# Performance work log

Hardware: AMD Instinct MI355X
Metric: run time of the kernel (lower is better)

Reference implementation:

```python
import jax, jax.numpy as jnp
import numpy as np

N = 100000   # nodes
E = 1600000  # edges (avg degree 16)
D = 64       # in_dim == emb_dim
L = 3        # num_layers
G = 2000     # graphs in batch
LN_EPS = 1e-5


def setup_inputs() -> dict:
    key = jax.random.key(0)
    ks = jax.random.split(key, 14)
    s = 0.05  # xavier-ish small init scale
    x = jax.random.normal(ks[0], (N, D), jnp.float32)
    edge_index = jax.random.randint(ks[1], (2, E), 0, N, dtype=jnp.int32)
    batch = jnp.sort(jax.random.randint(ks[2], (N,), 0, G, dtype=jnp.int32))
    return {
        "x": x,
        "edge_index": edge_index,
        "batch": batch,
        # stacked per-layer GIN MLP params: Linear(D,D) -> SiLU -> Linear(D,D)
        "W1": jax.random.normal(ks[3], (L, D, D), jnp.float32) * s,
        "b1": jnp.zeros((L, D), jnp.float32),
        "W2": jax.random.normal(ks[4], (L, D, D), jnp.float32) * s,
        "b2": jnp.zeros((L, D), jnp.float32),
        "eps": jnp.zeros((L,), jnp.float32),  # trainable eps, init 0
        "ln_g": jnp.ones((L, D), jnp.float32),
        "ln_b": jnp.zeros((L, D), jnp.float32),
        # gate_nn: Linear(D, D//2) -> SiLU -> Linear(D//2, 1)
        "gw1": jax.random.normal(ks[5], (D, D // 2), jnp.float32) * s,
        "gb1": jnp.zeros((D // 2,), jnp.float32),
        "gw2": jax.random.normal(ks[6], (D // 2, 1), jnp.float32) * s,
        "gb2": jnp.zeros((1,), jnp.float32),
    }


def _layernorm(h, g, b):
    mu = jnp.mean(h, axis=-1, keepdims=True)
    var = jnp.mean(jnp.square(h - mu), axis=-1, keepdims=True)
    return (h - mu) * jax.lax.rsqrt(var + LN_EPS) * g + b


def reference(x, edge_index, batch, W1, b1, W2, b2, eps, ln_g, ln_b, gw1, gb1, gw2, gb2):
    src, dst = edge_index[0], edge_index[1]
    # ---- GIN layers (eval mode: dropout is identity) ----
    for l in range(L):
        agg = jax.ops.segment_sum(x[src], dst, num_segments=N)  # scatter-add of neighbor feats
        h = (1.0 + eps[l]) * x + agg                             # GIN update
        h = jax.nn.silu(h @ W1[l] + b1[l]) @ W2[l] + b2[l]       # 2-layer MLP
        x = _layernorm(h, ln_g[l], ln_b[l])
    # ---- GlobalAttention pooling ----
    gate = (jax.nn.silu(x @ gw1 + gb1) @ gw2 + gb2)[:, 0]        # [N]
    m = jax.ops.segment_max(gate, batch, num_segments=G)         # per-graph max for stability
    e = jnp.exp(gate - m[batch])
    denom = jax.ops.segment_sum(e, batch, num_segments=G)
    a = e / denom[batch]                                         # per-graph softmax
    out = jax.ops.segment_sum(a[:, None] * x, batch, num_segments=G)  # [G, D]
    return out
```

## Files before the change

### kernel.cpp

```cpp
#include <hip/hip_runtime.h>
#include <math.h>

#define NN 100000
#define NE 1600000
#define D 64
#define NG 2000
#define LN_EPS 1e-5f
#define NB ((NN + 255) / 256)
#define NBK NB
#define NTILE ((NN + 63) / 64)
#define EPB 6400
#define LSTR 72
#define WFRAG_MLP 24576
#define WFRAG_TOT 26624

typedef __attribute__((ext_vector_type(8))) short short8;
typedef __attribute__((ext_vector_type(4))) float floatx4;

__device__ __forceinline__ unsigned short f2bf(float f) {
    unsigned int u = __float_as_uint(f);
    u += 0x7FFF + ((u >> 16) & 1);
    return (unsigned short)(u >> 16);
}
__device__ __forceinline__ float bfu2f(unsigned short v) {
    return __uint_as_float(((unsigned int)v) << 16);
}

__global__ __launch_bounds__(256) void k_conv(const float* __restrict__ x,
                                              unsigned short* __restrict__ xb) {
    int i = blockIdx.x * 256 + threadIdx.x;
    xb[i] = f2bf(x[i]);
}

__global__ __launch_bounds__(256) void k_wprep(const float* __restrict__ W1,
                                               const float* __restrict__ W2,
                                               const float* __restrict__ gw1,
                                               unsigned short* __restrict__ wfrag) {
    int idx = blockIdx.x * 256 + threadIdx.x;
    if (idx < WFRAG_MLP) {
        int l = idx / 8192;
        int rem = idx % 8192;
        int mat = rem / 4096;
        int r2 = rem % 4096;
        int ks = r2 / 2048;
        int c = (r2 / 512) % 4;
        int lane = (r2 / 8) % 64;
        int j = r2 % 8;
        int n = lane & 15, q = lane >> 4;
        int k = ks * 32 + q * 8 + j;
        int col = c * 16 + n;
        const float* Wm = mat ? W2 : W1;
        wfrag[idx] = f2bf(Wm[l * 4096 + k * 64 + col]);
    } else if (idx < WFRAG_TOT) {
        int g = idx - WFRAG_MLP;
        int ks = g / 1024;
        int c = (g / 512) % 2;
        int lane = (g / 8) % 64;
        int j = g % 8;
        int n = lane & 15, q = lane >> 4;
        int k = ks * 32 + q * 8 + j;
        wfrag[idx] = f2bf(gw1[k * 32 + c * 16 + n]);
    }
}

__global__ __launch_bounds__(256) void k_bcount(const int* __restrict__ dst,
                                                int* __restrict__ btot) {
    __shared__ int lcnt[NBK];
    int e0 = blockIdx.x * EPB;
    int tid = threadIdx.x;
    for (int i = tid; i < NBK; i += 256) lcnt[i] = 0;
    __syncthreads();
    for (int k = 0; k < EPB; k += 256)
        atomicAdd(&lcnt[dst[e0 + k + tid] >> 8], 1);
    __syncthreads();
    for (int i = tid; i < NBK; i += 256) {
        int c = lcnt[i];
        if (c) atomicAdd(&btot[i], c);
    }
}

__global__ __launch_bounds__(512) void k_bscan(const int* __restrict__ btot,
                                               int* __restrict__ bbase) {
    __shared__ int s[512];
    int t = threadIdx.x;
    int v = (t < NB) ? btot[t] : 0;
    s[t] = v;
    __syncthreads();
    for (int off = 1; off < 512; off <<= 1) {
        int u = (t >= off) ? s[t - off] : 0;
        __syncthreads();
        s[t] += u;
        __syncthreads();
    }
    if (t < NB) bbase[t] = s[t] - v;
    if (t == NB - 1) bbase[NB] = s[t];
}

__global__ __launch_bounds__(512) void k_bcurinit(const int* __restrict__ bbase,
                                                  int* __restrict__ bcur,
                                                  int* __restrict__ row_ptr) {
    int b = threadIdx.x;
    if (b < NBK) bcur[b * 16] = bbase[b];
    if (b == 0) row_ptr[NN] = NE;
}

__global__ __launch_bounds__(256) void k_part(const int* __restrict__ src,
                                              const int* __restrict__ dst,
                                              int* __restrict__ bcur,
                                              unsigned int* __restrict__ tmp) {
    __shared__ int lcnt[NBK];
    __shared__ int lbase[NBK];
    __shared__ int sd[EPB];
    __shared__ int ss[EPB];
    int e0 = blockIdx.x * EPB;
    int tid = threadIdx.x;

    for (int i = tid; i < NBK; i += 256) lcnt[i] = 0;
    __syncthreads();

    for (int k = 0; k < EPB; k += 256) {
        int d = dst[e0 + k + tid];
        int s = src[e0 + k + tid];
        sd[k + tid] = d;
        ss[k + tid] = s;
        atomicAdd(&lcnt[d >> 8], 1);
    }
    __syncthreads();

    for (int i = tid; i < NBK; i += 256) {
        int c = lcnt[i];
        lbase[i] = c ? atomicAdd(&bcur[i * 16], c) : 0;
        lcnt[i] = 0;
    }
    __syncthreads();

    for (int k = 0; k < EPB; k += 256) {
        int d = sd[k + tid];
        int s = ss[k + tid];
        int b = d >> 8;
        int pos = lbase[b] + atomicAdd(&lcnt[b], 1);
        tmp[pos] = ((unsigned int)s << 8) | (unsigned int)(d & 255);
    }
}

__global__ __launch_bounds__(256) void k_bfill(const unsigned int* __restrict__ tmp,
                                               const int* __restrict__ bbase,
                                               int* __restrict__ row_ptr,
                                               int* __restrict__ col) {
    __shared__ int lcur[256];
    __shared__ int wsum[4];
    int b = blockIdx.x;
    int nb0 = b * 256;
    int nodes = min(256, NN - nb0);
    int tid = threadIdx.x;
    int lane = tid & 63;
    int w = tid >> 6;
    int estart = bbase[b], eend = bbase[b + 1];

    lcur[tid] = 0;
    __syncthreads();
    for (int e = estart + tid; e < eend; e += 256)
        atomicAdd(&lcur[tmp[e] & 255], 1);
    __syncthreads();

    int v = lcur[tid];
    int x = v;
#pragma unroll
    for (int off = 1; off < 64; off <<= 1) {
        int u = __shfl_up(x, off, 64);
        if (lane >= off) x += u;
    }
    if (lane == 63) wsum[w] = x;
    __syncthreads();
    int base = estart;
    for (int k = 0; k < w; k++) base += wsum[k];
    int rp = base + x - v;
    if (tid < nodes) row_ptr[nb0 + tid] = rp;
    lcur[tid] = rp;
    __syncthreads();

    for (int e = estart + tid; e < eend; e += 256) {
        unsigned int p = tmp[e];
        int pos = atomicAdd(&lcur[p & 255], 1);
        col[pos] = (int)(p >> 8);
    }
}

__global__ __launch_bounds__(256) void k_gather(const unsigned short* __restrict__ xin,
                                                unsigned short* __restrict__ h,
                                                const int* __restrict__ row_ptr,
                                                const int* __restrict__ col,
                                                const float* __restrict__ epsp) {
    int w = threadIdx.x >> 6;
    int lane = threadIdx.x & 63;
    int g = lane >> 4;
    int fl = lane & 15;
    int node = (blockIdx.x * 4 + w) * 4 + g;
    int start = row_ptr[node], end = row_ptr[node + 1];

    float4 A0 = {0, 0, 0, 0}, A1 = {0, 0, 0, 0}, A2 = {0, 0, 0, 0}, A3 = {0, 0, 0, 0};
    int eb = start;
    for (; eb + 16 <= end; eb += 16) {
        int c = col[eb + fl];
        ushort4 v[16];
#pragma unroll
        for (int j = 0; j < 16; j++) {
            int idx = __shfl(c, g * 16 + j, 64);
            v[j] = *(const ushort4*)(xin + ((size_t)idx << 6) + fl * 4);
        }
#pragma unroll
        for (int j = 0; j < 16; j += 4) {
            A0.x += bfu2f(v[j].x); A0.y += bfu2f(v[j].y); A0.z += bfu2f(v[j].z); A0.w += bfu2f(v[j].w);
            A1.x += bfu2f(v[j+1].x); A1.y += bfu2f(v[j+1].y); A1.z += bfu2f(v[j+1].z); A1.w += bfu2f(v[j+1].w);
            A2.x += bfu2f(v[j+2].x); A2.y += bfu2f(v[j+2].y); A2.z += bfu2f(v[j+2].z); A2.w += bfu2f(v[j+2].w);
            A3.x += bfu2f(v[j+3].x); A3.y += bfu2f(v[j+3].y); A3.z += bfu2f(v[j+3].z); A3.w += bfu2f(v[j+3].w);
        }
    }
    if (eb < end) {
        int cnt = end - eb;
        int c = (fl < cnt) ? col[eb + fl] : 0;
        int j = 0;
        for (; j + 4 <= cnt; j += 4) {
            int i0 = __shfl(c, g * 16 + j, 64);
            int i1 = __shfl(c, g * 16 + j + 1, 64);
            int i2 = __shfl(c, g * 16 + j + 2, 64);
            int i3 = __shfl(c, g * 16 + j + 3, 64);
            ushort4 v0 = *(const ushort4*)(xin + ((size_t)i0 << 6) + fl * 4);
            ushort4 v1 = *(const ushort4*)(xin + ((size_t)i1 << 6) + fl * 4);
            ushort4 v2 = *(const ushort4*)(xin + ((size_t)i2 << 6) + fl * 4);
            ushort4 v3 = *(const ushort4*)(xin + ((size_t)i3 << 6) + fl * 4);
            A0.x += bfu2f(v0.x); A0.y += bfu2f(v0.y); A0.z += bfu2f(v0.z); A0.w += bfu2f(v0.w);
            A1.x += bfu2f(v1.x); A1.y += bfu2f(v1.y); A1.z += bfu2f(v1.z); A1.w += bfu2f(v1.w);
            A2.x += bfu2f(v2.x); A2.y += bfu2f(v2.y); A2.z += bfu2f(v2.z); A2.w += bfu2f(v2.w);
            A3.x += bfu2f(v3.x); A3.y += bfu2f(v3.y); A3.z += bfu2f(v3.z); A3.w += bfu2f(v3.w);
        }
        for (; j < cnt; j++) {
            int i0 = __shfl(c, g * 16 + j, 64);
            ushort4 v0 = *(const ushort4*)(xin + ((size_t)i0 << 6) + fl * 4);
            A0.x += bfu2f(v0.x); A0.y += bfu2f(v0.y); A0.z += bfu2f(v0.z); A0.w += bfu2f(v0.w);
        }
    }
    float ev = 1.0f + *epsp;
    ushort4 xs = *(const ushort4*)(xin + ((size_t)node << 6) + fl * 4);
    ushort4 o;
    o.x = f2bf(ev * bfu2f(xs.x) + ((A0.x + A1.x) + (A2.x + A3.x)));
    o.y = f2bf(ev * bfu2f(xs.y) + ((A0.y + A1.y) + (A2.y + A3.y)));
    o.z = f2bf(ev * bfu2f(xs.z) + ((A0.z + A1.z) + (A2.z + A3.z)));
    o.w = f2bf(ev * bfu2f(xs.w) + ((A0.w + A1.w) + (A2.w + A3.w)));
    *(ushort4*)(h + ((size_t)node << 6) + fl * 4) = o;
}

template <int LAST>
__global__ __launch_bounds__(256) void k_mfma(const unsigned short* __restrict__ h,
                                              unsigned short* __restrict__ xout,
                                              const short8* __restrict__ wf,
                                              const short8* __restrict__ gf,
                                              const float* __restrict__ b1,
                                              const float* __restrict__ b2,
                                              const float* __restrict__ lng,
                                              const float* __restrict__ lnb,
                                              const float* __restrict__ gb1,
                                              const float* __restrict__ gw2,
                                              const float* __restrict__ gb2,
                                              float* __restrict__ gate) {
    __shared__ __align__(16) unsigned short a2[4][16 * LSTR];
    int w = threadIdx.x >> 6;
    int lane = threadIdx.x & 63;
    int n = lane & 15;
    int q = lane >> 4;
    int base = blockIdx.x * 64 + w * 16;

    short8 B1f[2][4], B2f[2][4];
#pragma unroll
    for (int ks = 0; ks < 2; ks++)
#pragma unroll
        for (int c = 0; c < 4; c++) {
            B1f[ks][c] = wf[(ks * 4 + c) * 64 + lane];
            B2f[ks][c] = wf[512 + (ks * 4 + c) * 64 + lane];
        }
    short8 B3f[2][2];
    if (LAST) {
#pragma unroll
        for (int ks = 0; ks < 2; ks++)
#pragma unroll
            for (int c = 0; c < 2; c++)
                B3f[ks][c] = gf[(ks * 2 + c) * 64 + lane];
    }

    float b1v[4], b2v[4], lgv[4], lbv[4];
#pragma unroll
    for (int c = 0; c < 4; c++) {
        b1v[c] = b1[c * 16 + n];
        b2v[c] = b2[c * 16 + n];
        lgv[c] = lng[c * 16 + n];
        lbv[c] = lnb[c * 16 + n];
    }
    float gb1v[2], gw2v[2], gb2v = 0.f;
    if (LAST) {
        gb1v[0] = gb1[n]; gb1v[1] = gb1[16 + n];
        gw2v[0] = gw2[n]; gw2v[1] = gw2[16 + n];
        gb2v = gb2[0];
    }

    unsigned short* aw = a2[w];

    int mnode = base + n;
    int mc = min(mnode, NN - 1);
    const short8* hp = (const short8*)(h + ((size_t)mc << 6));
    short8 A0 = hp[q];
    short8 A1 = hp[4 + q];

    floatx4 acc1[4];
#pragma unroll
    for (int c = 0; c < 4; c++) {
        floatx4 a = {b1v[c], b1v[c], b1v[c], b1v[c]};
        a = __builtin_amdgcn_mfma_f32_16x16x32_bf16(A0, B1f[0][c], a, 0, 0, 0);
        a = __builtin_amdgcn_mfma_f32_16x16x32_bf16(A1, B1f[1][c], a, 0, 0, 0);
        acc1[c] = a;
    }

#pragma unroll
    for (int c = 0; c < 4; c++)
#pragma unroll
        for (int r = 0; r < 4; r++) {
            float v = acc1[c][r];
            v = v / (1.0f + __expf(-v));
            aw[(q * 4 + r) * LSTR + c * 16 + n] = f2bf(v);
        }

    const short8* ap = (const short8*)(aw + n * LSTR);
    short8 A20 = ap[q];
    short8 A21 = ap[4 + q];

    floatx4 acc2[4];
#pragma unroll
    for (int c = 0; c < 4; c++) {
        floatx4 a = {b2v[c], b2v[c], b2v[c], b2v[c]};
        a = __builtin_amdgcn_mfma_f32_16x16x32_bf16(A20, B2f[0][c], a, 0, 0, 0);
        a = __builtin_amdgcn_mfma_f32_16x16x32_bf16(A21, B2f[1][c], a, 0, 0, 0);
        acc2[c] = a;
    }

    float mu[4], inv[4];
#pragma unroll
    for (int r = 0; r < 4; r++) {
        float s = acc2[0][r] + acc2[1][r] + acc2[2][r] + acc2[3][r];
#pragma unroll
        for (int off = 1; off < 16; off <<= 1) s += __shfl_xor(s, off, 64);
        mu[r] = s * (1.0f / 64.0f);
        float d0 = acc2[0][r] - mu[r], d1 = acc2[1][r] - mu[r];
        float d2 = acc2[2][r] - mu[r], d3 = acc2[3][r] - mu[r];
        float vv = d0 * d0 + d1 * d1 + d2 * d2 + d3 * d3;
#pragma unroll
        for (int off = 1; off < 16; off <<= 1) vv += __shfl_xor(vv, off, 64);
        inv[r] = rsqrtf(vv * (1.0f / 64.0f) + LN_EPS);
    }

#pragma unroll
    for (int c = 0; c < 4; c++)
#pragma unroll
        for (int r = 0; r < 4; r++) {
            int node = base + q * 4 + r;
            float o = (acc2[c][r] - mu[r]) * inv[r] * lgv[c] + lbv[c];
            unsigned short ob = f2bf(o);
            if (node < NN) xout[((size_t)node << 6) + c * 16 + n] = ob;
            if (LAST) aw[(q * 4 + r) * LSTR + c * 16 + n] = ob;
        }

    if (LAST) {
        const short8* gp = (const short8*)(aw + n * LSTR);
        short8 G0 = gp[q];
        short8 G1 = gp[4 + q];
        floatx4 acc3[2];
#pragma unroll
        for (int c = 0; c < 2; c++) {
            floatx4 a = {gb1v[c], gb1v[c], gb1v[c], gb1v[c]};
            a = __builtin_amdgcn_mfma_f32_16x16x32_bf16(G0, B3f[0][c], a, 0, 0, 0);
            a = __builtin_amdgcn_mfma_f32_16x16x32_bf16(G1, B3f[1][c], a, 0, 0, 0);
            acc3[c] = a;
        }
#pragma unroll
        for (int r = 0; r < 4; r++) {
            float v0 = acc3[0][r];
            v0 = v0 / (1.0f + __expf(-v0));
            float v1 = acc3[1][r];
            v1 = v1 / (1.0f + __expf(-v1));
            float gsum = v0 * gw2v[0] + v1 * gw2v[1];
#pragma unroll
            for (int off = 1; off < 16; off <<= 1) gsum += __shfl_xor(gsum, off, 64);
            int node = base + q * 4 + r;
            if (n == 0 && node < NN) gate[node] = gsum + gb2v;
        }
    }
}

__global__ __launch_bounds__(256) void k_pool(const unsigned short* __restrict__ xf,
                                              const float* __restrict__ gate,
                                              const int* __restrict__ batch,
                                              float* __restrict__ out) {
    __shared__ float redm[4];
    __shared__ float reds[4];
    __shared__ float racc[4][D];
    int g = blockIdx.x;
    int w = threadIdx.x >> 6;
    int lane = threadIdx.x & 63;

    int lo = 0, hi = NN;
    while (lo < hi) { int mid = (lo + hi) >> 1; if (batch[mid] < g) lo = mid + 1; else hi = mid; }
    int start = lo;
    hi = NN;
    while (lo < hi) { int mid = (lo + hi) >> 1; if (batch[mid] < g + 1) lo = mid + 1; else hi = mid; }
    int end = lo;

    if (start >= end) {
        if (w == 0) out[((size_t)g << 6) + lane] = 0.0f;
        return;
    }

    float m = -INFINITY;
    for (int i = start + (int)threadIdx.x; i < end; i += 256) m = fmaxf(m, gate[i]);
#pragma unroll
    for (int mm = 32; mm >= 1; mm >>= 1) m = fmaxf(m, __shfl_xor(m, mm, 64));
    if (lane == 0) redm[w] = m;
    __syncthreads();
    m = fmaxf(fmaxf(redm[0], redm[1]), fmaxf(redm[2], redm[3]));

    float s = 0.0f;
    for (int i = start + (int)threadIdx.x; i < end; i += 256) s += __expf(gate[i] - m);
#pragma unroll
    for (int mm = 32; mm >= 1; mm >>= 1) s += __shfl_xor(s, mm, 64);
    if (lane == 0) reds[w] = s;
    __syncthreads();
    s = (reds[0] + reds[1]) + (reds[2] + reds[3]);

    float acc = 0.0f;
    for (int i = start + w; i < end; i += 4)
        acc += __expf(gate[i] - m) * bfu2f(xf[((size_t)i << 6) + lane]);
    racc[w][lane] = acc;
    __syncthreads();
    if (w == 0)
        out[((size_t)g << 6) + lane] =
            ((racc[0][lane] + racc[1][lane]) + (racc[2][lane] + racc[3][lane])) / s;
}

extern "C" void kernel_launch(void* const* d_in, const int* in_sizes, int n_in,
                              void* d_out, int out_size, void* d_ws, size_t ws_size,
                              hipStream_t stream) {
    const float* x   = (const float*)d_in[0];
    const int* ei    = (const int*)d_in[1];
    const int* batch = (const int*)d_in[2];
    const float* W1  = (const float*)d_in[3];
    const float* b1  = (const float*)d_in[4];
    const float* W2  = (const float*)d_in[5];
    const float* b2  = (const float*)d_in[6];
    const float* eps = (const float*)d_in[7];
    const float* lng = (const float*)d_in[8];
    const float* lnb = (const float*)d_in[9];
    const float* gw1 = (const float*)d_in[10];
    const float* gb1 = (const float*)d_in[11];
    const float* gw2 = (const float*)d_in[12];
    const float* gb2 = (const float*)d_in[13];

    const int* src = ei;
    const int* dst = ei + NE;

    unsigned short* xb    = (unsigned short*)d_ws;
    unsigned short* h     = xb + (size_t)NN * D;
    float* gate           = (float*)(h + (size_t)NN * D);
    int* row_ptr          = (int*)(gate + NN);
    int* col              = row_ptr + NN + 1;
    unsigned int* tmp     = (unsigned int*)(col + NE);
    int* btot             = (int*)(tmp + NE);
    int* bbase            = btot + NB;
    int* bcur             = bbase + NB + 1;
    unsigned short* wfrag = (unsigned short*)(bcur + NBK * 16);

    float* out = (float*)d_out;

    hipMemsetAsync(btot, 0, (size_t)NB * sizeof(int), stream);
    k_conv<<<(NN * D) / 256, 256, 0, stream>>>(x, xb);
    k_wprep<<<WFRAG_TOT / 256, 256, 0, stream>>>(W1, W2, gw1, wfrag);
    k_bcount<<<NE / EPB, 256, 0, stream>>>(dst, btot);
    k_bscan<<<1, 512, 0, stream>>>(btot, bbase);
    k_bcurinit<<<1, 512, 0, stream>>>(bbase, bcur, row_ptr);
    k_part<<<NE / EPB, 256, 0, stream>>>(src, dst, bcur, tmp);
    k_bfill<<<NBK, 256, 0, stream>>>(tmp, bbase, row_ptr, col);

    const short8* wf0 = (const short8*)(wfrag);
    const short8* wf1 = (const short8*)(wfrag + 8192);
    const short8* wf2 = (const short8*)(wfrag + 16384);
    const short8* gf  = (const short8*)(wfrag + WFRAG_MLP);

    k_gather<<<NN / 16, 256, 0, stream>>>(xb, h, row_ptr, col, eps + 0);
    k_mfma<0><<<NTILE, 256, 0, stream>>>(h, xb, wf0, gf,
        b1 + 0 * D, b2 + 0 * D, lng + 0 * D, lnb + 0 * D, gb1, gw2, gb2, gate);

    k_gather<<<NN / 16, 256, 0, stream>>>(xb, h, row_ptr, col, eps + 1);
    k_mfma<0><<<NTILE, 256, 0, stream>>>(h, xb, wf1, gf,
        b1 + 1 * D, b2 + 1 * D, lng + 1 * D, lnb + 1 * D, gb1, gw2, gb2, gate);

    k_gather<<<NN / 16, 256, 0, stream>>>(xb, h, row_ptr, col, eps + 2);
    k_mfma<1><<<NTILE, 256, 0, stream>>>(h, xb, wf2, gf,
        b1 + 2 * D, b2 + 2 * D, lng + 2 * D, lnb + 2 * D, gb1, gw2, gb2, gate);

    k_pool<<<NG, 256, 0, stream>>>(xb, gate, batch, out);
}
```

Measured before the change: 336.6 us.

## Fuse neighbor gather into MLP layer kernel and drop fp32-to-bf16 conversion pass

Merges the per-layer gather/aggregate kernel into the MFMA MLP kernel. Aggregated rows are written to shared memory instead of a global h buffer, and output ping-pongs between two bf16 buffers. The first layer gathers directly from fp32 x, which removes the separate conversion kernel. The bcur init is folded into the scan kernel. Together these cut launches and the global round trip of h, but the first layer now gathers twice as many bytes per edge, and gathers run with only 4 nodes per wave-group per iteration, which may lower memory-level parallelism.

```diff
diff --git a/kernel.cpp b/kernel.cpp
--- a/kernel.cpp
+++ b/kernel.cpp
@@ -24,12 +24,6 @@
 }
 __device__ __forceinline__ float bfu2f(unsigned short v) {
     return __uint_as_float(((unsigned int)v) << 16);
-}
-
-__global__ __launch_bounds__(256) void k_conv(const float* __restrict__ x,
-                                              unsigned short* __restrict__ xb) {
-    int i = blockIdx.x * 256 + threadIdx.x;
-    xb[i] = f2bf(x[i]);
 }
 
 __global__ __launch_bounds__(256) void k_wprep(const float* __restrict__ W1,
@@ -80,7 +74,9 @@
 }
 
 __global__ __launch_bounds__(512) void k_bscan(const int* __restrict__ btot,
-                                               int* __restrict__ bbase) {
+                                               int* __restrict__ bbase,
+                                               int* __restrict__ bcur,
+                                               int* __restrict__ row_ptr) {
     __shared__ int s[512];
     int t = threadIdx.x;
     int v = (t < NB) ? btot[t] : 0;
@@ -92,16 +88,12 @@
         s[t] += u;
         __syncthreads();
     }
-    if (t < NB) bbase[t] = s[t] - v;
+    if (t < NB) {
+        bbase[t] = s[t] - v;
+        bcur[t * 16] = s[t] - v;
+    }
     if (t == NB - 1) bbase[NB] = s[t];
-}
-
-__global__ __launch_bounds__(512) void k_bcurinit(const int* __restrict__ bbase,
-                                                  int* __restrict__ bcur,
-                                                  int* __restrict__ row_ptr) {
-    int b = threadIdx.x;
-    if (b < NBK) bcur[b * 16] = bbase[b];
-    if (b == 0) row_ptr[NN] = NE;
+    if (t == 0) row_ptr[NN] = NE;
 }
 
 __global__ __launch_bounds__(256) void k_part(const int* __restrict__ src,
@@ -186,89 +178,106 @@
     }
 }
 
-__global__ __launch_bounds__(256) void k_gather(const unsigned short* __restrict__ xin,
-                                                unsigned short* __restrict__ h,
-                                                const int* __restrict__ row_ptr,
-                                                const int* __restrict__ col,
-                                                const float* __restrict__ epsp) {
-    int w = threadIdx.x >> 6;
-    int lane = threadIdx.x & 63;
-    int g = lane >> 4;
-    int fl = lane & 15;
-    int node = (blockIdx.x * 4 + w) * 4 + g;
-    int start = row_ptr[node], end = row_ptr[node + 1];
-
-    float4 A0 = {0, 0, 0, 0}, A1 = {0, 0, 0, 0}, A2 = {0, 0, 0, 0}, A3 = {0, 0, 0, 0};
-    int eb = start;
-    for (; eb + 16 <= end; eb += 16) {
-        int c = col[eb + fl];
-        ushort4 v[16];
-#pragma unroll
-        for (int j = 0; j < 16; j++) {
-            int idx = __shfl(c, g * 16 + j, 64);
-            v[j] = *(const ushort4*)(xin + ((size_t)idx << 6) + fl * 4);
-        }
-#pragma unroll
-        for (int j = 0; j < 16; j += 4) {
-            A0.x += bfu2f(v[j].x); A0.y += bfu2f(v[j].y); A0.z += bfu2f(v[j].z); A0.w += bfu2f(v[j].w);
-            A1.x += bfu2f(v[j+1].x); A1.y += bfu2f(v[j+1].y); A1.z += bfu2f(v[j+1].z); A1.w += bfu2f(v[j+1].w);
-            A2.x += bfu2f(v[j+2].x); A2.y += bfu2f(v[j+2].y); A2.z += bfu2f(v[j+2].z); A2.w += bfu2f(v[j+2].w);
-            A3.x += bfu2f(v[j+3].x); A3.y += bfu2f(v[j+3].y); A3.z += bfu2f(v[j+3].z); A3.w += bfu2f(v[j+3].w);
-        }
-    }
-    if (eb < end) {
-        int cnt = end - eb;
-        int c = (fl < cnt) ? col[eb + fl] : 0;
-        int j = 0;
-        for (; j + 4 <= cnt; j += 4) {
-            int i0 = __shfl(c, g * 16 + j, 64);
-            int i1 = __shfl(c, g * 16 + j + 1, 64);
-            int i2 = __shfl(c, g * 16 + j + 2, 64);
-            int i3 = __shfl(c, g * 16 + j + 3, 64);
-            ushort4 v0 = *(const ushort4*)(xin + ((size_t)i0 << 6) + fl * 4);
-            ushort4 v1 = *(const ushort4*)(xin + ((size_t)i1 << 6) + fl * 4);
-            ushort4 v2 = *(const ushort4*)(xin + ((size_t)i2 << 6) + fl * 4);
-            ushort4 v3 = *(const ushort4*)(xin + ((size_t)i3 << 6) + fl * 4);
-            A0.x += bfu2f(v0.x); A0.y += bfu2f(v0.y); A0.z += bfu2f(v0.z); A0.w += bfu2f(v0.w);
-            A1.x += bfu2f(v1.x); A1.y += bfu2f(v1.y); A1.z += bfu2f(v1.z); A1.w += bfu2f(v1.w);
-            A2.x += bfu2f(v2.x); A2.y += bfu2f(v2.y); A2.z += bfu2f(v2.z); A2.w += bfu2f(v2.w);
-            A3.x += bfu2f(v3.x); A3.y += bfu2f(v3.y); A3.z += bfu2f(v3.z); A3.w += bfu2f(v3.w);
-        }
-        for (; j < cnt; j++) {
-            int i0 = __shfl(c, g * 16 + j, 64);
-            ushort4 v0 = *(const ushort4*)(xin + ((size_t)i0 << 6) + fl * 4);
-            A0.x += bfu2f(v0.x); A0.y += bfu2f(v0.y); A0.z += bfu2f(v0.z); A0.w += bfu2f(v0.w);
-        }
-    }
-    float ev = 1.0f + *epsp;
-    ushort4 xs = *(const ushort4*)(xin + ((size_t)node << 6) + fl * 4);
-    ushort4 o;
-    o.x = f2bf(ev * bfu2f(xs.x) + ((A0.x + A1.x) + (A2.x + A3.x)));
-    o.y = f2bf(ev * bfu2f(xs.y) + ((A0.y + A1.y) + (A2.y + A3.y)));
-    o.z = f2bf(ev * bfu2f(xs.z) + ((A0.z + A1.z) + (A2.z + A3.z)));
-    o.w = f2bf(ev * bfu2f(xs.w) + ((A0.w + A1.w) + (A2.w + A3.w)));
-    *(ushort4*)(h + ((size_t)node << 6) + fl * 4) = o;
-}
-
-template <int LAST>
-__global__ __launch_bounds__(256) void k_mfma(const unsigned short* __restrict__ h,
-                                              unsigned short* __restrict__ xout,
-                                              const short8* __restrict__ wf,
-                                              const short8* __restrict__ gf,
-                                              const float* __restrict__ b1,
-                                              const float* __restrict__ b2,
-                                              const float* __restrict__ lng,
-                                              const float* __restrict__ lnb,
-                                              const float* __restrict__ gb1,
-                                              const float* __restrict__ gw2,
-                                              const float* __restrict__ gb2,
-                                              float* __restrict__ gate) {
+template <int FIRST, int LAST>
+__global__ __launch_bounds__(256) void k_layer(const float* __restrict__ xf32,
+                                               const unsigned short* __restrict__ xbf,
+                                               unsigned short* __restrict__ xout,
+                                               const int* __restrict__ row_ptr,
+                                               const int* __restrict__ col,
+                                               const float* __restrict__ epsp,
+                                               const short8* __restrict__ wf,
+                                               const short8* __restrict__ gf,
+                                               const float* __restrict__ b1,
+                                               const float* __restrict__ b2,
+                                               const float* __restrict__ lng,
+                                               const float* __restrict__ lnb,
+                                               const float* __restrict__ gb1,
+                                               const float* __restrict__ gw2,
+                                               const float* __restrict__ gb2,
+                                               float* __restrict__ gate) {
     __shared__ __align__(16) unsigned short a2[4][16 * LSTR];
     int w = threadIdx.x >> 6;
     int lane = threadIdx.x & 63;
     int n = lane & 15;
     int q = lane >> 4;
+    int g = q;
+    int fl = n;
     int base = blockIdx.x * 64 + w * 16;
+    unsigned short* aw = a2[w];
+
+    float ev = 1.0f + *epsp;
+
+    for (int sub = 0; sub < 4; sub++) {
+        int node = base + sub * 4 + g;
+        int nc = min(node, NN - 1);
+        int start = row_ptr[nc], end = row_ptr[nc + 1];
+
+        float4 A0 = {0, 0, 0, 0}, A1 = {0, 0, 0, 0}, A2 = {0, 0, 0, 0}, A3 = {0, 0, 0, 0};
+        int eb = start;
+        for (; eb + 16 <= end; eb += 16) {
+            int c = col[eb + fl];
+            if (FIRST) {
+#pragma unroll
+                for (int half = 0; half < 2; half++) {
+                    float4 v[8];
+#pragma unroll
+                    for (int j = 0; j < 8; j++) {
+                        int idx = __shfl(c, g * 16 + half * 8 + j, 64);
+                        v[j] = *(const float4*)(xf32 + ((size_t)idx << 6) + fl * 4);
+                    }
+#pragma unroll
+                    for (int j = 0; j < 8; j += 4) {
+                        A0.x += v[j].x;   A0.y += v[j].y;   A0.z += v[j].z;   A0.w += v[j].w;
+                        A1.x += v[j+1].x; A1.y += v[j+1].y; A1.z += v[j+1].z; A1.w += v[j+1].w;
+                        A2.x += v[j+2].x; A2.y += v[j+2].y; A2.z += v[j+2].z; A2.w += v[j+2].w;
+                        A3.x += v[j+3].x; A3.y += v[j+3].y; A3.z += v[j+3].z; A3.w += v[j+3].w;
+                    }
+                }
+            } else {
+                ushort4 v[16];
+#pragma unroll
+                for (int j = 0; j < 16; j++) {
+                    int idx = __shfl(c, g * 16 + j, 64);
+                    v[j] = *(const ushort4*)(xbf + ((size_t)idx << 6) + fl * 4);
+                }
+#pragma unroll
+                for (int j = 0; j < 16; j += 4) {
+                    A0.x += bfu2f(v[j].x);   A0.y += bfu2f(v[j].y);   A0.z += bfu2f(v[j].z);   A0.w += bfu2f(v[j].w);
+                    A1.x += bfu2f(v[j+1].x); A1.y += bfu2f(v[j+1].y); A1.z += bfu2f(v[j+1].z); A1.w += bfu2f(v[j+1].w);
+                    A2.x += bfu2f(v[j+2].x); A2.y += bfu2f(v[j+2].y); A2.z += bfu2f(v[j+2].z); A2.w += bfu2f(v[j+2].w);
+                    A3.x += bfu2f(v[j+3].x); A3.y += bfu2f(v[j+3].y); A3.z += bfu2f(v[j+3].z); A3.w += bfu2f(v[j+3].w);
+                }
+            }
+        }
+        if (eb < end) {
+            int cnt = end - eb;
+            int c = (fl < cnt) ? col[eb + fl] : 0;
+            for (int j = 0; j < cnt; j++) {
+                int idx = __shfl(c, g * 16 + j, 64);
+                if (FIRST) {
+                    float4 v0 = *(const float4*)(xf32 + ((size_t)idx << 6) + fl * 4);
+                    A0.x += v0.x; A0.y += v0.y; A0.z += v0.z; A0.w += v0.w;
+                } else {
+                    ushort4 v0 = *(const ushort4*)(xbf + ((size_t)idx << 6) + fl * 4);
+                    A0.x += bfu2f(v0.x); A0.y += bfu2f(v0.y); A0.z += bfu2f(v0.z); A0.w += bfu2f(v0.w);
+                }
+            }
+        }
+        float sx, sy, sz, sw;
+        if (FIRST) {
+            float4 xs = *(const float4*)(xf32 + ((size_t)nc << 6) + fl * 4);
+            sx = xs.x; sy = xs.y; sz = xs.z; sw = xs.w;
+        } else {
+            ushort4 xs = *(const ushort4*)(xbf + ((size_t)nc << 6) + fl * 4);
+            sx = bfu2f(xs.x); sy = bfu2f(xs.y); sz = bfu2f(xs.z); sw = bfu2f(xs.w);
+        }
+        ushort4 o;
+        o.x = f2bf(ev * sx + ((A0.x + A1.x) + (A2.x + A3.x)));
+        o.y = f2bf(ev * sy + ((A0.y + A1.y) + (A2.y + A3.y)));
+        o.z = f2bf(ev * sz + ((A0.z + A1.z) + (A2.z + A3.z)));
+        o.w = f2bf(ev * sw + ((A0.w + A1.w) + (A2.w + A3.w)));
+        *(ushort4*)(aw + (sub * 4 + g) * LSTR + fl * 4) = o;
+    }
 
     short8 B1f[2][4], B2f[2][4];
 #pragma unroll
@@ -302,13 +311,9 @@
         gb2v = gb2[0];
     }
 
-    unsigned short* aw = a2[w];
-
-    int mnode = base + n;
-    int mc = min(mnode, NN - 1);
-    const short8* hp = (const short8*)(h + ((size_t)mc << 6));
-    short8 A0 = hp[q];
-    short8 A1 = hp[4 + q];
+    const short8* ap = (const short8*)(aw + n * LSTR);
+    short8 A0 = ap[q];
+    short8 A1 = ap[4 + q];
 
     floatx4 acc1[4];
 #pragma unroll
@@ -328,7 +333,6 @@
             aw[(q * 4 + r) * LSTR + c * 16 + n] = f2bf(v);
         }
 
-    const short8* ap = (const short8*)(aw + n * LSTR);
     short8 A20 = ap[q];
     short8 A21 = ap[4 + q];
 
@@ -368,9 +372,8 @@
         }
 
     if (LAST) {
-        const short8* gp = (const short8*)(aw + n * LSTR);
-        short8 G0 = gp[q];
-        short8 G1 = gp[4 + q];
+        short8 G0 = ap[q];
+        short8 G1 = ap[4 + q];
         floatx4 acc3[2];
 #pragma unroll
         for (int c = 0; c < 2; c++) {
@@ -464,9 +467,9 @@
     const int* src = ei;
     const int* dst = ei + NE;
 
-    unsigned short* xb    = (unsigned short*)d_ws;
-    unsigned short* h     = xb + (size_t)NN * D;
-    float* gate           = (float*)(h + (size_t)NN * D);
+    unsigned short* xa    = (unsigned short*)d_ws;
+    unsigned short* xbuf  = xa + (size_t)NN * D;
+    float* gate           = (float*)(xbuf + (size_t)NN * D);
     int* row_ptr          = (int*)(gate + NN);
     int* col              = row_ptr + NN + 1;
     unsigned int* tmp     = (unsigned int*)(col + NE);
@@ -478,11 +481,9 @@
     float* out = (float*)d_out;
 
     hipMemsetAsync(btot, 0, (size_t)NB * sizeof(int), stream);
-    k_conv<<<(NN * D) / 256, 256, 0, stream>>>(x, xb);
     k_wprep<<<WFRAG_TOT / 256, 256, 0, stream>>>(W1, W2, gw1, wfrag);
     k_bcount<<<NE / EPB, 256, 0, stream>>>(dst, btot);
-    k_bscan<<<1, 512, 0, stream>>>(btot, bbase);
-    k_bcurinit<<<1, 512, 0, stream>>>(bbase, bcur, row_ptr);
+    k_bscan<<<1, 512, 0, stream>>>(btot, bbase, bcur, row_ptr);
     k_part<<<NE / EPB, 256, 0, stream>>>(src, dst, bcur, tmp);
     k_bfill<<<NBK, 256, 0, stream>>>(tmp, bbase, row_ptr, col);
 
@@ -491,17 +492,12 @@
     const short8* wf2 = (const short8*)(wfrag + 16384);
     const short8* gf  = (const short8*)(wfrag + WFRAG_MLP);
 
-    k_gather<<<NN / 16, 256, 0, stream>>>(xb, h, row_ptr, col, eps + 0);
-    k_mfma<0><<<NTILE, 256, 0, stream>>>(h, xb, wf0, gf,
-        b1 + 0 * D, b2 + 0 * D, lng + 0 * D, lnb + 0 * D, gb1, gw2, gb2, gate);
-
-    k_gather<<<NN / 16, 256, 0, stream>>>(xb, h, row_ptr, col, eps + 1);
-    k_mfma<0><<<NTILE, 256, 0, stream>>>(h, xb, wf1, gf,
-        b1 + 1 * D, b2 + 1 * D, lng + 1 * D, lnb + 1 * D, gb1, gw2, gb2, gate);
-
-    k_gather<<<NN / 16, 256, 0, stream>>>(xb, h, row_ptr, col, eps + 2);
-    k_mfma<1><<<NTILE, 256, 0, stream>>>(h, xb, wf2, gf,
-        b1 + 2 * D, b2 + 2 * D, lng + 2 * D, lnb + 2 * D, gb1, gw2, gb2, gate);
-
-    k_pool<<<NG, 256, 0, stream>>>(xb, gate, batch, out);
-}
+    k_layer<1, 0><<<NTILE, 256, 0, stream>>>(x, nullptr, xa, row_ptr, col, eps + 0,
+        wf0, gf, b1 + 0 * D, b2 + 0 * D, lng + 0 * D, lnb + 0 * D, gb1, gw2, gb2, gate);
+    k_layer<0, 0><<<NTILE, 256, 0, stream>>>(nullptr, xa, xbuf, row_ptr, col, eps + 1,
+        wf1, gf, b1 + 1 * D, b2 + 1 * D, lng + 1 * D, lnb + 1 * D, gb1, gw2, gb2, gate);
+    k_layer<0, 1><<<NTILE, 256, 0, stream>>>(nullptr, xbuf, xa, row_ptr, col, eps + 2,
+        wf2, gf, b1 + 2 * D, b2 + 2 * D, lng + 2 * D, lnb + 2 * D, gb1, gw2, gb2, gate);
+
+    k_pool<<<NG, 256, 0, stream>>>(xa, gate, batch, out);
+}
```

Result: slower. 452.4 us (+34.4%).

## Build CSR with fixed-capacity buckets, dropping the count and scan passes

Applied to the files above, without the earlier changes.

Replaces the count / scan / partition / fill CSR construction with fixed-capacity per-bucket regions (CAP slots per 256-node bucket). This removes the dst counting kernel, the scan kernel, the memset and their launches. The fill kernel now stages each bucket in shared memory and sorts it in place, writing separate start and end row pointers that the gather kernel reads. It relies on no bucket exceeding CAP edges, which holds for uniform random graphs but could overflow on skewed degree distributions. A small edit also reuses an existing LDS pointer for the gate MFMA operands.

```diff
diff --git a/kernel.cpp b/kernel.cpp
--- a/kernel.cpp
+++ b/kernel.cpp
@@ -10,6 +10,7 @@
 #define NBK NB
 #define NTILE ((NN + 63) / 64)
 #define EPB 6400
+#define CAP 6144
 #define LSTR 72
 #define WFRAG_MLP 24576
 #define WFRAG_TOT 26624
@@ -63,51 +64,15 @@
     }
 }
 
-__global__ __launch_bounds__(256) void k_bcount(const int* __restrict__ dst,
-                                                int* __restrict__ btot) {
-    __shared__ int lcnt[NBK];
-    int e0 = blockIdx.x * EPB;
-    int tid = threadIdx.x;
-    for (int i = tid; i < NBK; i += 256) lcnt[i] = 0;
-    __syncthreads();
-    for (int k = 0; k < EPB; k += 256)
-        atomicAdd(&lcnt[dst[e0 + k + tid] >> 8], 1);
-    __syncthreads();
-    for (int i = tid; i < NBK; i += 256) {
-        int c = lcnt[i];
-        if (c) atomicAdd(&btot[i], c);
-    }
-}
-
-__global__ __launch_bounds__(512) void k_bscan(const int* __restrict__ btot,
-                                               int* __restrict__ bbase) {
-    __shared__ int s[512];
-    int t = threadIdx.x;
-    int v = (t < NB) ? btot[t] : 0;
-    s[t] = v;
-    __syncthreads();
-    for (int off = 1; off < 512; off <<= 1) {
-        int u = (t >= off) ? s[t - off] : 0;
-        __syncthreads();
-        s[t] += u;
-        __syncthreads();
-    }
-    if (t < NB) bbase[t] = s[t] - v;
-    if (t == NB - 1) bbase[NB] = s[t];
-}
-
-__global__ __launch_bounds__(512) void k_bcurinit(const int* __restrict__ bbase,
-                                                  int* __restrict__ bcur,
-                                                  int* __restrict__ row_ptr) {
+__global__ __launch_bounds__(512) void k_init(int* __restrict__ bcur) {
     int b = threadIdx.x;
-    if (b < NBK) bcur[b * 16] = bbase[b];
-    if (b == 0) row_ptr[NN] = NE;
+    if (b < NBK) bcur[b * 16] = b * CAP;
 }
 
 __global__ __launch_bounds__(256) void k_part(const int* __restrict__ src,
                                               const int* __restrict__ dst,
                                               int* __restrict__ bcur,
-                                              unsigned int* __restrict__ tmp) {
+                                              unsigned int* __restrict__ colbuf) {
     __shared__ int lcnt[NBK];
     __shared__ int lbase[NBK];
     __shared__ int sd[EPB];
@@ -139,28 +104,32 @@
         int s = ss[k + tid];
         int b = d >> 8;
         int pos = lbase[b] + atomicAdd(&lcnt[b], 1);
-        tmp[pos] = ((unsigned int)s << 8) | (unsigned int)(d & 255);
-    }
-}
-
-__global__ __launch_bounds__(256) void k_bfill(const unsigned int* __restrict__ tmp,
-                                               const int* __restrict__ bbase,
-                                               int* __restrict__ row_ptr,
-                                               int* __restrict__ col) {
+        colbuf[pos] = ((unsigned int)s << 8) | (unsigned int)(d & 255);
+    }
+}
+
+__global__ __launch_bounds__(256) void k_bfill(unsigned int* __restrict__ colbuf,
+                                               const int* __restrict__ bcur,
+                                               int* __restrict__ rps,
+                                               int* __restrict__ rpe) {
+    __shared__ unsigned int sld[CAP];
     __shared__ int lcur[256];
     __shared__ int wsum[4];
     int b = blockIdx.x;
+    int ebase = b * CAP;
+    int cnt = bcur[b * 16] - ebase;
     int nb0 = b * 256;
     int nodes = min(256, NN - nb0);
     int tid = threadIdx.x;
     int lane = tid & 63;
     int w = tid >> 6;
-    int estart = bbase[b], eend = bbase[b + 1];
-
+
+    for (int e = tid; e < cnt; e += 256) sld[e] = colbuf[ebase + e];
     lcur[tid] = 0;
     __syncthreads();
-    for (int e = estart + tid; e < eend; e += 256)
-        atomicAdd(&lcur[tmp[e] & 255], 1);
+
+    for (int e = tid; e < cnt; e += 256)
+        atomicAdd(&lcur[sld[e] & 255], 1);
     __syncthreads();
 
     int v = lcur[tid];
@@ -172,23 +141,27 @@
     }
     if (lane == 63) wsum[w] = x;
     __syncthreads();
-    int base = estart;
+    int base = ebase;
     for (int k = 0; k < w; k++) base += wsum[k];
     int rp = base + x - v;
-    if (tid < nodes) row_ptr[nb0 + tid] = rp;
+    if (tid < nodes) {
+        rps[nb0 + tid] = rp;
+        rpe[nb0 + tid] = rp + v;
+    }
     lcur[tid] = rp;
     __syncthreads();
 
-    for (int e = estart + tid; e < eend; e += 256) {
-        unsigned int p = tmp[e];
+    for (int e = tid; e < cnt; e += 256) {
+        unsigned int p = sld[e];
         int pos = atomicAdd(&lcur[p & 255], 1);
-        col[pos] = (int)(p >> 8);
+        colbuf[pos] = p >> 8;
     }
 }
 
 __global__ __launch_bounds__(256) void k_gather(const unsigned short* __restrict__ xin,
                                                 unsigned short* __restrict__ h,
-                                                const int* __restrict__ row_ptr,
+                                                const int* __restrict__ rps,
+                                                const int* __restrict__ rpe,
                                                 const int* __restrict__ col,
                                                 const float* __restrict__ epsp) {
     int w = threadIdx.x >> 6;
@@ -196,7 +169,7 @@
     int g = lane >> 4;
     int fl = lane & 15;
     int node = (blockIdx.x * 4 + w) * 4 + g;
-    int start = row_ptr[node], end = row_ptr[node + 1];
+    int start = rps[node], end = rpe[node];
 
     float4 A0 = {0, 0, 0, 0}, A1 = {0, 0, 0, 0}, A2 = {0, 0, 0, 0}, A3 = {0, 0, 0, 0};
     int eb = start;
@@ -368,9 +341,8 @@
         }
 
     if (LAST) {
-        const short8* gp = (const short8*)(aw + n * LSTR);
-        short8 G0 = gp[q];
-        short8 G1 = gp[4 + q];
+        short8 G0 = ap[q];
+        short8 G1 = ap[4 + q];
         floatx4 acc3[2];
 #pragma unroll
         for (int c = 0; c < 2; c++) {
@@ -467,39 +439,34 @@
     unsigned short* xb    = (unsigned short*)d_ws;
     unsigned short* h     = xb + (size_t)NN * D;
     float* gate           = (float*)(h + (size_t)NN * D);
-    int* row_ptr          = (int*)(gate + NN);
-    int* col              = row_ptr + NN + 1;
-    unsigned int* tmp     = (unsigned int*)(col + NE);
-    int* btot             = (int*)(tmp + NE);
-    int* bbase            = btot + NB;
-    int* bcur             = bbase + NB + 1;
+    int* rps              = (int*)(gate + NN);
+    int* rpe              = rps + NN;
+    int* colbuf           = rpe + NN;
+    int* bcur             = colbuf + (size_t)NBK * CAP;
     unsigned short* wfrag = (unsigned short*)(bcur + NBK * 16);
 
     float* out = (float*)d_out;
 
-    hipMemsetAsync(btot, 0, (size_t)NB * sizeof(int), stream);
     k_conv<<<(NN * D) / 256, 256, 0, stream>>>(x, xb);
     k_wprep<<<WFRAG_TOT / 256, 256, 0, stream>>>(W1, W2, gw1, wfrag);
-    k_bcount<<<NE / EPB, 256, 0, stream>>>(dst, btot);
-    k_bscan<<<1, 512, 0, stream>>>(btot, bbase);
-    k_bcurinit<<<1, 512, 0, stream>>>(bbase, bcur, row_ptr);
-    k_part<<<NE / EPB, 256, 0, stream>>>(src, dst, bcur, tmp);
-    k_bfill<<<NBK, 256, 0, stream>>>(tmp, bbase, row_ptr, col);
+    k_init<<<1, 512, 0, stream>>>(bcur);
+    k_part<<<NE / EPB, 256, 0, stream>>>(src, dst, bcur, (unsigned int*)colbuf);
+    k_bfill<<<NBK, 256, 0, stream>>>((unsigned int*)colbuf, bcur, rps, rpe);
 
     const short8* wf0 = (const short8*)(wfrag);
     const short8* wf1 = (const short8*)(wfrag + 8192);
     const short8* wf2 = (const short8*)(wfrag + 16384);
     const short8* gf  = (const short8*)(wfrag + WFRAG_MLP);
 
-    k_gather<<<NN / 16, 256, 0, stream>>>(xb, h, row_ptr, col, eps + 0);
+    k_gather<<<NN / 16, 256, 0, stream>>>(xb, h, rps, rpe, colbuf, eps + 0);
     k_mfma<0><<<NTILE, 256, 0, stream>>>(h, xb, wf0, gf,
         b1 + 0 * D, b2 + 0 * D, lng + 0 * D, lnb + 0 * D, gb1, gw2, gb2, gate);
 
-    k_gather<<<NN / 16, 256, 0, stream>>>(xb, h, row_ptr, col, eps + 1);
+    k_gather<<<NN / 16, 256, 0, stream>>>(xb, h, rps, rpe, colbuf, eps + 1);
     k_mfma<0><<<NTILE, 256, 0, stream>>>(h, xb, wf1, gf,
         b1 + 1 * D, b2 + 1 * D, lng + 1 * D, lnb + 1 * D, gb1, gw2, gb2, gate);
 
-    k_gather<<<NN / 16, 256, 0, stream>>>(xb, h, row_ptr, col, eps + 2);
+    k_gather<<<NN / 16, 256, 0, stream>>>(xb, h, rps, rpe, colbuf, eps + 2);
     k_mfma<1><<<NTILE, 256, 0, stream>>>(h, xb, wf2, gf,
         b1 + 2 * D, b2 + 2 * D, lng + 2 * D, lnb + 2 * D, gb1, gw2, gb2, gate);
 
```

After: 314.4 us. 1.07x faster.
